# Optimization experiments

Hardware: AMD Instinct MI355X
Metric: run time of the kernel (lower is better)

Reference implementation:

```python
import jax, jax.numpy as jnp
import numpy as np

B = 64        # number of graph segments
BASE = 384    # mean verts per segment
LMAX = 512    # pad length (counts in [256, 512])
H_DIM = 256
H_DIV = 128   # h_dim // h_dim_div
HEADS = 4
DH = H_DIV // HEADS  # 32


def _counts(seed):
    rng = np.random.default_rng(seed)
    d = rng.integers(-128, 129, B)
    d[1::2] = -d[::2]            # paired so the total is exactly B*BASE
    return (BASE + d).astype(np.int64)


def _pad_indices(counts, L):
    # Gather indices/mask mapping packed ragged tokens -> padded [B, L].
    counts = np.asarray(counts)
    off = np.concatenate([[0], np.cumsum(counts)[:-1]])
    ar = np.arange(L)[None, :]
    mask = ar < counts[:, None]
    idx = np.where(mask, off[:, None] + ar, 0)
    return idx, mask


def setup_inputs() -> dict:
    key = jax.random.key(0)
    ks = jax.random.split(key, 16)
    src_num_verts = _counts(0)
    dst_num_verts = _counts(1)
    total = B * BASE  # 24576 for both src and dst

    def w(k, shape):
        return 0.02 * jax.random.normal(k, shape, jnp.float32)

    return {
        'src_h': jax.random.normal(ks[0], (total, H_DIM), jnp.float32),
        'dst_h': jax.random.normal(ks[1], (total, H_DIM), jnp.float32),
        'src_num_verts': src_num_verts,
        'dst_num_verts': dst_num_verts,
        # 1x1 Conv1d == linear over channels
        'Wq': w(ks[2], (H_DIV, H_DIM)), 'bq': w(ks[3], (H_DIV,)),
        'Wk': w(ks[4], (H_DIV, H_DIM)), 'bk': w(ks[5], (H_DIV,)),
        'Wv': w(ks[6], (H_DIV, H_DIM)), 'bv': w(ks[7], (H_DIV,)),
        'Wm': w(ks[8], (H_DIV, H_DIV)), 'bm': w(ks[9], (H_DIV,)),
        'W1': w(ks[10], (H_DIM, H_DIM + H_DIV)), 'b1': w(ks[11], (H_DIM,)),
        'g1': 1.0 + 0.1 * jax.random.normal(ks[12], (H_DIM,), jnp.float32),
        'be1': w(ks[13], (H_DIM,)),
        'rm1': w(ks[14], (H_DIM,)),
        'rv1': jax.random.uniform(ks[15], (H_DIM,), jnp.float32, 0.5, 1.5),
        'W2': w(jax.random.fold_in(key, 100), (H_DIM, H_DIM)),
        'b2': w(jax.random.fold_in(key, 101), (H_DIM,)),
        'g2': 1.0 + 0.1 * jax.random.normal(jax.random.fold_in(key, 102), (H_DIM,), jnp.float32),
        'be2': w(jax.random.fold_in(key, 103), (H_DIM,)),
        'rm2': w(jax.random.fold_in(key, 104), (H_DIM,)),
        'rv2': jax.random.uniform(jax.random.fold_in(key, 105), (H_DIM,), jnp.float32, 0.5, 1.5),
    }


def _bn(x, g, b, rm, rv):
    # BatchNorm1d in eval mode (running stats)
    return (x - rm) / jnp.sqrt(rv + 1e-5) * g + b


def reference(src_h, dst_h, src_num_verts, dst_num_verts,
              Wq, bq, Wk, bk, Wv, bv, Wm, bm,
              W1, b1, g1, be1, rm1, rv1,
              W2, b2, g2, be2, rm2, rv2):
    didx, dmask = _pad_indices(dst_num_verts, LMAX)
    sidx, smask = _pad_indices(src_num_verts, LMAX)

    # fused projections over all packed tokens (1x1 conv == matmul)
    q = src_h_proj = dst_h @ Wq.T + bq        # [Nd, H_DIV]
    k = src_h @ Wk.T + bk                     # [Ns, H_DIV]
    v = src_h @ Wv.T + bv

    # pad to block-diagonal batched form; channel c = d*HEADS + h per torch view
    qp = q[didx].reshape(B, LMAX, DH, HEADS)
    kp = k[sidx].reshape(B, LMAX, DH, HEADS)
    vp = v[sidx].reshape(B, LMAX, DH, HEADS)

    scores = jnp.einsum('bndh,bmdh->bhnm', qp, kp) / (DH ** 0.5)
    scores = jnp.where(jnp.asarray(smask)[:, None, None, :], scores, -1e9)
    attn = jax.nn.softmax(scores, axis=-1)
    msg = jnp.einsum('bhnm,bmdh->bndh', attn, vp).reshape(B, LMAX, H_DIV)
    msg = msg @ Wm.T + bm                     # merge conv

    bb, ii = np.nonzero(dmask)                # unpad back to packed layout
    h_msg = msg[bb, ii]                       # [Nd, H_DIV]

    x = jnp.concatenate([dst_h, h_msg], axis=-1)
    x = _bn(x @ W1.T + b1, g1, be1, rm1, rv1)
    x = jax.nn.relu(x)
    x = _bn(x @ W2.T + b2, g2, be2, rm2, rv2)
    return dst_h + x
```

## Files before the change

kernel.cpp:

```cpp
#include <hip/hip_runtime.h>
#include <hip/hip_bf16.h>
#include <math.h>

#define B_SEG 64
#define HDIM 256
#define HDIV 128
#define NHEADS 4
#define DH 32
#define KSTR 40
#define VSTR 520
#define PSTR 136
#define QSC 0.17677669529663687f

typedef unsigned short u16;
typedef unsigned int u32;

typedef __attribute__((ext_vector_type(8))) short s8v;
typedef __attribute__((ext_vector_type(4))) float f4v;

__device__ __forceinline__ u16 f2bf(float f) {
    u32 v;
    __builtin_memcpy(&v, &f, 4);
    u32 r = v + 0x7fffu + ((v >> 16) & 1u);
    return (u16)(r >> 16);
}

__device__ __forceinline__ void async_cp16(const u16* g, u16* l) {
    __builtin_amdgcn_global_load_lds(
        (const __attribute__((address_space(1))) u32*)g,
        (__attribute__((address_space(3))) u32*)l, 16, 0, 0);
}

__global__ __launch_bounds__(256) void k_prep(
    const float* __restrict__ Wq, const float* __restrict__ bq,
    const float* __restrict__ Wk, const float* __restrict__ bk,
    const float* __restrict__ Wv, const float* __restrict__ bv,
    const float* __restrict__ Wm, const float* __restrict__ bm,
    const float* __restrict__ W1, const float* __restrict__ b1,
    const float* __restrict__ g1, const float* __restrict__ be1,
    const float* __restrict__ rm1, const float* __restrict__ rv1,
    const float* __restrict__ W2, const float* __restrict__ b2,
    const float* __restrict__ g2, const float* __restrict__ be2,
    const float* __restrict__ rm2, const float* __restrict__ rv2,
    const int* __restrict__ sc_raw, const int* __restrict__ dc_raw,
    const float* __restrict__ src_h, const float* __restrict__ dst_h,
    int* __restrict__ meta,
    u16* __restrict__ pWq, u16* __restrict__ pWkv,
    u16* __restrict__ pW1f, u16* __restrict__ pW2,
    float* __restrict__ bqp, float* __restrict__ bkvp,
    float* __restrict__ sc1, float* __restrict__ sh1,
    float* __restrict__ sc2, float* __restrict__ sh2,
    u16* __restrict__ srcb, u16* __restrict__ dstb, int ntot) {
    if (blockIdx.x < 1028) {
        int idx = blockIdx.x * 256 + threadIdx.x;
        if (idx < 32768) {
            int cp = idx >> 8, k = idx & 255;
            int c = ((cp & 31) << 2) | (cp >> 5);
            pWq[idx] = f2bf(Wq[c * 256 + k]);
        } else if (idx < 98304) {
            int i = idx - 32768;
            int rp = i >> 8, k = i & 255;
            int r = rp & 127;
            int c = ((r & 31) << 2) | (r >> 5);
            float v = (rp < 128) ? Wk[c * 256 + k] : Wv[c * 256 + k];
            pWkv[i] = f2bf(v);
        } else if (idx < 163840) {
            int i = idx - 98304;
            int o = i >> 8, k = i & 255;
            pW1f[o * 384 + k] = f2bf(W1[o * 384 + k]);
        } else if (idx < 196608) {
            int i = idx - 163840;
            int o = i >> 7, cp = i & 127;
            int c = ((cp & 31) << 2) | (cp >> 5);
            float acc = 0.f;
            for (int j = 0; j < 128; j++)
                acc += W1[o * 384 + 256 + j] * Wm[j * 128 + c];
            pW1f[o * 384 + 256 + cp] = f2bf(acc);
        } else if (idx < 262144) {
            int i = idx - 196608;
            pW2[i] = f2bf(W2[i]);
        } else if (idx < 263168) {
            int p = idx - 262144;
            if (p < 128) {
                int c = ((p & 31) << 2) | (p >> 5);
                bqp[p] = bq[c] * QSC;
            } else if (p < 384) {
                int r = p - 128; int rr = r & 127;
                int c = ((rr & 31) << 2) | (rr >> 5);
                bkvp[r] = (r < 128) ? bk[c] : bv[c];
            } else if (p < 640) {
                int o = p - 384;
                float bsum = 0.f;
                for (int j = 0; j < 128; j++)
                    bsum += W1[o * 384 + 256 + j] * bm[j];
                float s = g1[o] * rsqrtf(rv1[o] + 1e-5f);
                sc1[o] = s;
                sh1[o] = (b1[o] + bsum - rm1[o]) * s + be1[o];
            } else if (p < 896) {
                int o = p - 640;
                float s = g2[o] * rsqrtf(rv2[o] + 1e-5f);
                sc2[o] = s;
                sh2[o] = (b2[o] - rm2[o]) * s + be2[o];
            }
        }
    } else if (blockIdx.x == 1028) {
        if (threadIdx.x == 0) {
            bool is64 = (sc_raw[1] == 0);
            int so = 0, dofs = 0;
            for (int i = 0; i < B_SEG; i++) {
                int s = is64 ? sc_raw[2 * i] : sc_raw[i];
                int d = is64 ? dc_raw[2 * i] : dc_raw[i];
                meta[i] = s; meta[64 + i] = d;
                meta[128 + i] = so; meta[192 + i] = dofs;
                so += s; dofs += d;
            }
        }
    } else {
        int i = (blockIdx.x - 1029) * 256 + threadIdx.x;
        int half = ntot * 64;
        const float4* s;
        u16* o;
        int j = i;
        if (i < half) { s = (const float4*)src_h; o = srcb; }
        else { s = (const float4*)dst_h; o = dstb; j = i - half; }
        float4 v = s[j];
        ushort4 u = {f2bf(v.x), f2bf(v.y), f2bf(v.z), f2bf(v.w)};
        ((ushort4*)o)[j] = u;
    }
}

__device__ __forceinline__ void gemm_body(
    const u16* __restrict__ A, int lda,
    const u16* __restrict__ A2, int lda2, int K1,
    const u16* __restrict__ Bw, int K, int m0, int n0,
    const float* __restrict__ scale, const float* __restrict__ shift,
    const float* __restrict__ resid,
    void* __restrict__ Cout, int ldc, int flags,
    u16* Al, u16* Bl) {
    int tid = threadIdx.x;
    int w = tid >> 6, lane = tid & 63;
    int wm = w & 1, wn = w >> 1;
    int l15 = lane & 15, quad = lane >> 4;
    int srow = w * 32 + (lane >> 2);
    int scol = (lane & 3) << 3;
    u16* al0 = Al + w * 1024;
    u16* bl0 = Bl + w * 1024;
    f4v acc[4][4] = {};

    for (int k0 = 0; k0 < K; k0 += 32) {
        const u16* Ag; int aL, acol;
        if (k0 < K1) { Ag = A; aL = lda; acol = k0; }
        else { Ag = A2; aL = lda2; acol = k0 - K1; }
        async_cp16(&Ag[(size_t)(m0 + srow) * aL + acol + scol], al0);
        async_cp16(&Ag[(size_t)(m0 + srow + 16) * aL + acol + scol], al0 + 512);
        async_cp16(&Bw[(size_t)(n0 + srow) * K + k0 + scol], bl0);
        async_cp16(&Bw[(size_t)(n0 + srow + 16) * K + k0 + scol], bl0 + 512);
        __syncthreads();
        s8v af[4], bf[4];
#pragma unroll
        for (int i = 0; i < 4; i++)
            af[i] = *(const s8v*)(&Al[(wm * 64 + i * 16 + l15) * 32 + quad * 8]);
#pragma unroll
        for (int j = 0; j < 4; j++)
            bf[j] = *(const s8v*)(&Bl[(wn * 64 + j * 16 + l15) * 32 + quad * 8]);
#pragma unroll
        for (int i = 0; i < 4; i++)
#pragma unroll
            for (int j = 0; j < 4; j++)
                acc[i][j] = __builtin_amdgcn_mfma_f32_16x16x32_bf16(
                    af[i], bf[j], acc[i][j], 0, 0, 0);
        __syncthreads();
    }
#pragma unroll
    for (int i = 0; i < 4; i++) {
#pragma unroll
        for (int j = 0; j < 4; j++) {
            int n = n0 + wn * 64 + j * 16 + l15;
            float sc = scale ? scale[n] : 1.f;
            float sh = shift ? shift[n] : 0.f;
#pragma unroll
            for (int r = 0; r < 4; r++) {
                int m = m0 + wm * 64 + i * 16 + quad * 4 + r;
                float v = acc[i][j][r];
                if (flags & 4) v *= QSC;
                v = v * sc + sh;
                if (flags & 1) v = fmaxf(v, 0.f);
                if (resid) v += resid[(size_t)m * 256 + n];
                if (flags & 2) ((float*)Cout)[(size_t)m * ldc + n] = v;
                else ((u16*)Cout)[(size_t)m * ldc + n] = f2bf(v);
            }
        }
    }
}

__global__ __launch_bounds__(256) void k_qkv(
    const u16* __restrict__ dstb, const u16* __restrict__ srcb,
    const u16* __restrict__ pWq, const u16* __restrict__ pWkv,
    const float* __restrict__ bqp, const float* __restrict__ bkvp,
    u16* __restrict__ qb, u16* __restrict__ kvb) {
    __shared__ u16 Al[4096];
    __shared__ u16 Bl[4096];
    int m0 = blockIdx.x * 128;
    if (blockIdx.y == 0)
        gemm_body(dstb, 256, dstb, 256, 256, pWq, 256, m0, 0,
                  nullptr, bqp, nullptr, qb, 128, 4, Al, Bl);
    else
        gemm_body(srcb, 256, srcb, 256, 256, pWkv, 256, m0, (blockIdx.y - 1) * 128,
                  nullptr, bkvp, nullptr, kvb, 256, 0, Al, Bl);
}

__global__ __launch_bounds__(256) void k_gemm(
    const u16* __restrict__ A, int lda,
    const u16* __restrict__ A2, int lda2, int K1,
    const u16* __restrict__ Bw, int K,
    const float* __restrict__ scale, const float* __restrict__ shift,
    const float* __restrict__ resid,
    void* __restrict__ Cout, int ldc, int flags) {
    __shared__ u16 Al[4096];
    __shared__ u16 Bl[4096];
    gemm_body(A, lda, A2, lda2, K1, Bw, K, blockIdx.x * 128, blockIdx.y * 128,
              scale, shift, resid, Cout, ldc, flags, Al, Bl);
}

__global__ __launch_bounds__(512, 2) void k_attn(
    const u16* __restrict__ qb, const u16* __restrict__ kvb,
    const int* __restrict__ meta, u16* __restrict__ msgb) {
    extern __shared__ u16 sm[];
    u16* Kl = sm;
    u16* Vl = sm + 512 * KSTR;
    u16* Pl = Vl + 32 * VSTR;
    int b = blockIdx.x, h = blockIdx.y;
    int ns = meta[b], nd = meta[64 + b];
    int soff = meta[128 + b], doff = meta[192 + b];
    int tid = threadIdx.x, w = tid >> 6, lane = tid & 63;
    int l15 = lane & 15, quad = lane >> 4;

    {
        int m = tid;
        if (m < ns) {
            const uint4* ks = (const uint4*)&kvb[(size_t)(soff + m) * 256 + h * 32];
#pragma unroll
            for (int q4 = 0; q4 < 4; q4++)
                *(uint4*)&Kl[m * KSTR + q4 * 8] = ks[q4];
            uint4 vv[4];
            const uint4* vs = (const uint4*)&kvb[(size_t)(soff + m) * 256 + 128 + h * 32];
#pragma unroll
            for (int q4 = 0; q4 < 4; q4++) vv[q4] = vs[q4];
            const u16* pv = (const u16*)vv;
#pragma unroll
            for (int d = 0; d < 32; d++) Vl[d * VSTR + m] = pv[d];
        } else {
#pragma unroll
            for (int d = 0; d < 32; d++) Vl[d * VSTR + m] = 0;
        }
    }
    __syncthreads();

    int nt = (ns + 15) >> 4;
    int nc = (ns + 127) >> 7;
    u16* Pw = Pl + w * 16 * PSTR;

    for (int s0 = w * 16; s0 < nd; s0 += 128) {
        int qr = min(s0 + l15, nd - 1);
        s8v aq = *(const s8v*)&qb[(size_t)(doff + qr) * 128 + h * 32 + quad * 8];

        f4v e[32];
        float lsum[4] = {0.f, 0.f, 0.f, 0.f};
#pragma unroll
        for (int t = 0; t < 32; t++) {
            if (t < nt) {
                int kr = t * 16 + l15;
                s8v bk = *(const s8v*)&Kl[kr * KSTR + quad * 8];
                f4v s_ = __builtin_amdgcn_mfma_f32_16x16x32_bf16(
                    aq, bk, (f4v){0.f, 0.f, 0.f, 0.f}, 0, 0, 0);
                bool ok = kr < ns;
#pragma unroll
                for (int r = 0; r < 4; r++) {
                    float ev = ok ? __expf(s_[r]) : 0.f;
                    e[t][r] = ev;
                    lsum[r] += ev;
                }
            } else {
#pragma unroll
                for (int r = 0; r < 4; r++) e[t][r] = 0.f;
            }
        }
        float inv[4];
#pragma unroll
        for (int r = 0; r < 4; r++) {
            float s_ = lsum[r];
#pragma unroll
            for (int x = 1; x < 16; x <<= 1) s_ += __shfl_xor(s_, x, 16);
            inv[r] = 1.f / s_;
        }

        f4v oa0 = {0.f, 0.f, 0.f, 0.f}, oa1 = {0.f, 0.f, 0.f, 0.f};
#pragma unroll
        for (int c = 0; c < 4; c++) {
            if (c < nc) {
#pragma unroll
                for (int tt = 0; tt < 8; tt++)
#pragma unroll
                    for (int r = 0; r < 4; r++)
                        Pw[(quad * 4 + r) * PSTR + tt * 16 + l15] =
                            f2bf(e[c * 8 + tt][r]);
#pragma unroll
                for (int kc = 0; kc < 4; kc++) {
                    s8v ap = *(const s8v*)&Pw[l15 * PSTR + kc * 32 + quad * 8];
                    s8v bv0 = *(const s8v*)&Vl[l15 * VSTR + c * 128 + kc * 32 + quad * 8];
                    s8v bv1 = *(const s8v*)&Vl[(16 + l15) * VSTR + c * 128 + kc * 32 + quad * 8];
                    oa0 = __builtin_amdgcn_mfma_f32_16x16x32_bf16(ap, bv0, oa0, 0, 0, 0);
                    oa1 = __builtin_amdgcn_mfma_f32_16x16x32_bf16(ap, bv1, oa1, 0, 0, 0);
                }
            }
        }
#pragma unroll
        for (int r = 0; r < 4; r++) {
            int row = s0 + quad * 4 + r;
            if (row < nd) {
                size_t base = (size_t)(doff + row) * 128 + h * 32;
                msgb[base + l15] = f2bf(oa0[r] * inv[r]);
                msgb[base + 16 + l15] = f2bf(oa1[r] * inv[r]);
            }
        }
    }
}

extern "C" void kernel_launch(void* const* d_in, const int* in_sizes, int n_in,
                              void* d_out, int out_size, void* d_ws, size_t ws_size,
                              hipStream_t stream) {
    const float* src_h = (const float*)d_in[0];
    const float* dst_h = (const float*)d_in[1];
    const int* snv = (const int*)d_in[2];
    const int* dnv = (const int*)d_in[3];
    const float* Wq = (const float*)d_in[4];  const float* bq = (const float*)d_in[5];
    const float* Wk = (const float*)d_in[6];  const float* bk = (const float*)d_in[7];
    const float* Wv = (const float*)d_in[8];  const float* bv = (const float*)d_in[9];
    const float* Wm = (const float*)d_in[10]; const float* bm = (const float*)d_in[11];
    const float* W1 = (const float*)d_in[12]; const float* b1 = (const float*)d_in[13];
    const float* g1 = (const float*)d_in[14]; const float* be1 = (const float*)d_in[15];
    const float* rm1 = (const float*)d_in[16]; const float* rv1 = (const float*)d_in[17];
    const float* W2 = (const float*)d_in[18]; const float* b2 = (const float*)d_in[19];
    const float* g2 = (const float*)d_in[20]; const float* be2 = (const float*)d_in[21];
    const float* rm2 = (const float*)d_in[22]; const float* rv2 = (const float*)d_in[23];

    int ntot = out_size / HDIM;
    int mt = ntot / 128;

    char* ws = (char*)d_ws;
    int* meta = (int*)ws;
    float* bqp = (float*)(ws + 4096);
    float* bkvp = (float*)(ws + 4608);
    float* sc1 = (float*)(ws + 6144);
    float* sh1 = (float*)(ws + 7168);
    float* sc2 = (float*)(ws + 8192);
    float* sh2 = (float*)(ws + 9216);
    u16* pWq = (u16*)(ws + 16384);
    u16* pWkv = (u16*)(ws + 81920);
    u16* pW1f = (u16*)(ws + 212992);
    u16* pW2 = (u16*)(ws + 409600);
    u16* srcb = (u16*)(ws + 1048576);
    u16* x1b = srcb;
    u16* dstb = (u16*)(ws + 13631488);

    u16* qb = (u16*)d_out;
    u16* kvb = qb + (size_t)ntot * 128;
    u16* msgb = kvb + (size_t)ntot * 256;

    hipFuncSetAttribute((const void*)k_attn,
                        hipFuncAttributeMaxDynamicSharedMemorySize, 131072);

    k_prep<<<dim3(1029 + ntot / 2), dim3(256), 0, stream>>>(
        Wq, bq, Wk, bk, Wv, bv, Wm, bm, W1, b1, g1, be1, rm1, rv1,
        W2, b2, g2, be2, rm2, rv2, snv, dnv, src_h, dst_h, meta,
        pWq, pWkv, pW1f, pW2, bqp, bkvp, sc1, sh1, sc2, sh2,
        srcb, dstb, ntot);
    k_qkv<<<dim3(mt, 3), dim3(256), 0, stream>>>(
        dstb, srcb, pWq, pWkv, bqp, bkvp, qb, kvb);
    k_attn<<<dim3(B_SEG, NHEADS), dim3(512), 109056, stream>>>(qb, kvb, meta, msgb);
    k_gemm<<<dim3(mt, 2), dim3(256), 0, stream>>>(
        dstb, 256, msgb, 128, 256, pW1f, 384, sc1, sh1, nullptr, x1b, 256, 1);
    k_gemm<<<dim3(mt, 2), dim3(256), 0, stream>>>(
        x1b, 256, x1b, 256, 256, pW2, 256, sc2, sh2, dst_h, d_out, 256, 2);
}
```

Baseline: 235.6 us.

## Split attention across query halves, stream K from global, widen GEMM K-step

The attention kernel gains a third grid dimension that splits each segment's query tiles across two blocks. K is no longer staged in LDS and is read directly from global memory, which shrinks shared memory so more blocks fit per CU. The score, exp and PV work is fused per 128-key chunk, so only 8 score tiles stay live in registers instead of 32. Separately, the GEMM body now loads a 64-wide K slab per barrier pair to halve synchronisations, at the cost of doubling its LDS footprint.

```diff
diff --git a/kernel.cpp b/kernel.cpp
--- a/kernel.cpp
+++ b/kernel.cpp
@@ -7,7 +7,6 @@
 #define HDIV 128
 #define NHEADS 4
 #define DH 32
-#define KSTR 40
 #define VSTR 520
 #define PSTR 136
 #define QSC 0.17677669529663687f
@@ -141,34 +140,40 @@
     int w = tid >> 6, lane = tid & 63;
     int wm = w & 1, wn = w >> 1;
     int l15 = lane & 15, quad = lane >> 4;
-    int srow = w * 32 + (lane >> 2);
-    int scol = (lane & 3) << 3;
-    u16* al0 = Al + w * 1024;
-    u16* bl0 = Bl + w * 1024;
+    int srow = w * 32 + (lane >> 3);
+    int scol = (lane & 7) << 3;
     f4v acc[4][4] = {};
 
-    for (int k0 = 0; k0 < K; k0 += 32) {
+    for (int k0 = 0; k0 < K; k0 += 64) {
         const u16* Ag; int aL, acol;
         if (k0 < K1) { Ag = A; aL = lda; acol = k0; }
         else { Ag = A2; aL = lda2; acol = k0 - K1; }
-        async_cp16(&Ag[(size_t)(m0 + srow) * aL + acol + scol], al0);
-        async_cp16(&Ag[(size_t)(m0 + srow + 16) * aL + acol + scol], al0 + 512);
-        async_cp16(&Bw[(size_t)(n0 + srow) * K + k0 + scol], bl0);
-        async_cp16(&Bw[(size_t)(n0 + srow + 16) * K + k0 + scol], bl0 + 512);
+#pragma unroll
+        for (int j = 0; j < 4; j++) {
+            async_cp16(&Ag[(size_t)(m0 + srow + j * 8) * aL + acol + scol],
+                       Al + w * 2048 + j * 512);
+            async_cp16(&Bw[(size_t)(n0 + srow + j * 8) * K + k0 + scol],
+                       Bl + w * 2048 + j * 512);
+        }
         __syncthreads();
-        s8v af[4], bf[4];
-#pragma unroll
-        for (int i = 0; i < 4; i++)
-            af[i] = *(const s8v*)(&Al[(wm * 64 + i * 16 + l15) * 32 + quad * 8]);
-#pragma unroll
-        for (int j = 0; j < 4; j++)
-            bf[j] = *(const s8v*)(&Bl[(wn * 64 + j * 16 + l15) * 32 + quad * 8]);
-#pragma unroll
-        for (int i = 0; i < 4; i++)
+#pragma unroll
+        for (int kk = 0; kk < 2; kk++) {
+            s8v af[4], bf[4];
+#pragma unroll
+            for (int i = 0; i < 4; i++)
+                af[i] = *(const s8v*)(&Al[(wm * 64 + i * 16 + l15) * 64
+                                          + kk * 32 + quad * 8]);
 #pragma unroll
             for (int j = 0; j < 4; j++)
-                acc[i][j] = __builtin_amdgcn_mfma_f32_16x16x32_bf16(
-                    af[i], bf[j], acc[i][j], 0, 0, 0);
+                bf[j] = *(const s8v*)(&Bl[(wn * 64 + j * 16 + l15) * 64
+                                          + kk * 32 + quad * 8]);
+#pragma unroll
+            for (int i = 0; i < 4; i++)
+#pragma unroll
+                for (int j = 0; j < 4; j++)
+                    acc[i][j] = __builtin_amdgcn_mfma_f32_16x16x32_bf16(
+                        af[i], bf[j], acc[i][j], 0, 0, 0);
+        }
         __syncthreads();
     }
 #pragma unroll
@@ -198,8 +203,8 @@
     const u16* __restrict__ pWq, const u16* __restrict__ pWkv,
     const float* __restrict__ bqp, const float* __restrict__ bkvp,
     u16* __restrict__ qb, u16* __restrict__ kvb) {
-    __shared__ u16 Al[4096];
-    __shared__ u16 Bl[4096];
+    __shared__ u16 Al[8192];
+    __shared__ u16 Bl[8192];
     int m0 = blockIdx.x * 128;
     if (blockIdx.y == 0)
         gemm_body(dstb, 256, dstb, 256, 256, pWq, 256, m0, 0,
@@ -216,20 +221,19 @@
     const float* __restrict__ scale, const float* __restrict__ shift,
     const float* __restrict__ resid,
     void* __restrict__ Cout, int ldc, int flags) {
-    __shared__ u16 Al[4096];
-    __shared__ u16 Bl[4096];
+    __shared__ u16 Al[8192];
+    __shared__ u16 Bl[8192];
     gemm_body(A, lda, A2, lda2, K1, Bw, K, blockIdx.x * 128, blockIdx.y * 128,
               scale, shift, resid, Cout, ldc, flags, Al, Bl);
 }
 
-__global__ __launch_bounds__(512, 2) void k_attn(
+__global__ __launch_bounds__(512, 4) void k_attn(
     const u16* __restrict__ qb, const u16* __restrict__ kvb,
     const int* __restrict__ meta, u16* __restrict__ msgb) {
     extern __shared__ u16 sm[];
-    u16* Kl = sm;
-    u16* Vl = sm + 512 * KSTR;
-    u16* Pl = Vl + 32 * VSTR;
-    int b = blockIdx.x, h = blockIdx.y;
+    u16* Vl = sm;
+    u16* Pl = sm + 32 * VSTR;
+    int b = blockIdx.x, h = blockIdx.y, z = blockIdx.z;
     int ns = meta[b], nd = meta[64 + b];
     int soff = meta[128 + b], doff = meta[192 + b];
     int tid = threadIdx.x, w = tid >> 6, lane = tid & 63;
@@ -238,12 +242,9 @@
     {
         int m = tid;
         if (m < ns) {
-            const uint4* ks = (const uint4*)&kvb[(size_t)(soff + m) * 256 + h * 32];
-#pragma unroll
-            for (int q4 = 0; q4 < 4; q4++)
-                *(uint4*)&Kl[m * KSTR + q4 * 8] = ks[q4];
             uint4 vv[4];
-            const uint4* vs = (const uint4*)&kvb[(size_t)(soff + m) * 256 + 128 + h * 32];
+            const uint4* vs =
+                (const uint4*)&kvb[(size_t)(soff + m) * 256 + 128 + h * 32];
 #pragma unroll
             for (int q4 = 0; q4 < 4; q4++) vv[q4] = vs[q4];
             const u16* pv = (const u16*)vv;
@@ -256,54 +257,43 @@
     }
     __syncthreads();
 
-    int nt = (ns + 15) >> 4;
     int nc = (ns + 127) >> 7;
     u16* Pw = Pl + w * 16 * PSTR;
-
-    for (int s0 = w * 16; s0 < nd; s0 += 128) {
+    const u16* kb = kvb + h * 32;
+
+    for (int s0 = (z * 8 + w) * 16; s0 < nd; s0 += 256) {
         int qr = min(s0 + l15, nd - 1);
         s8v aq = *(const s8v*)&qb[(size_t)(doff + qr) * 128 + h * 32 + quad * 8];
 
-        f4v e[32];
         float lsum[4] = {0.f, 0.f, 0.f, 0.f};
-#pragma unroll
-        for (int t = 0; t < 32; t++) {
-            if (t < nt) {
-                int kr = t * 16 + l15;
-                s8v bk = *(const s8v*)&Kl[kr * KSTR + quad * 8];
-                f4v s_ = __builtin_amdgcn_mfma_f32_16x16x32_bf16(
-                    aq, bk, (f4v){0.f, 0.f, 0.f, 0.f}, 0, 0, 0);
-                bool ok = kr < ns;
-#pragma unroll
-                for (int r = 0; r < 4; r++) {
-                    float ev = ok ? __expf(s_[r]) : 0.f;
-                    e[t][r] = ev;
-                    lsum[r] += ev;
-                }
-            } else {
-#pragma unroll
-                for (int r = 0; r < 4; r++) e[t][r] = 0.f;
-            }
-        }
-        float inv[4];
-#pragma unroll
-        for (int r = 0; r < 4; r++) {
-            float s_ = lsum[r];
-#pragma unroll
-            for (int x = 1; x < 16; x <<= 1) s_ += __shfl_xor(s_, x, 16);
-            inv[r] = 1.f / s_;
-        }
-
         f4v oa0 = {0.f, 0.f, 0.f, 0.f}, oa1 = {0.f, 0.f, 0.f, 0.f};
 #pragma unroll
         for (int c = 0; c < 4; c++) {
             if (c < nc) {
+                f4v e[8];
+#pragma unroll
+                for (int tt = 0; tt < 8; tt++) {
+                    int kr = min(c * 128 + tt * 16 + l15, ns - 1);
+                    s8v bk = *(const s8v*)&kb[(size_t)(soff + kr) * 256 + quad * 8];
+                    e[tt] = __builtin_amdgcn_mfma_f32_16x16x32_bf16(
+                        aq, bk, (f4v){0.f, 0.f, 0.f, 0.f}, 0, 0, 0);
+                }
+#pragma unroll
+                for (int tt = 0; tt < 8; tt++) {
+                    bool ok = (c * 128 + tt * 16 + l15) < ns;
+#pragma unroll
+                    for (int r = 0; r < 4; r++) {
+                        float ev = ok ? __expf(e[tt][r]) : 0.f;
+                        e[tt][r] = ev;
+                        lsum[r] += ev;
+                    }
+                }
 #pragma unroll
                 for (int tt = 0; tt < 8; tt++)
 #pragma unroll
                     for (int r = 0; r < 4; r++)
                         Pw[(quad * 4 + r) * PSTR + tt * 16 + l15] =
-                            f2bf(e[c * 8 + tt][r]);
+                            f2bf(e[tt][r]);
 #pragma unroll
                 for (int kc = 0; kc < 4; kc++) {
                     s8v ap = *(const s8v*)&Pw[l15 * PSTR + kc * 32 + quad * 8];
@@ -313,6 +303,14 @@
                     oa1 = __builtin_amdgcn_mfma_f32_16x16x32_bf16(ap, bv1, oa1, 0, 0, 0);
                 }
             }
+        }
+        float inv[4];
+#pragma unroll
+        for (int r = 0; r < 4; r++) {
+            float s_ = lsum[r];
+#pragma unroll
+            for (int x = 1; x < 16; x <<= 1) s_ += __shfl_xor(s_, x, 16);
+            inv[r] = 1.f / s_;
         }
 #pragma unroll
         for (int r = 0; r < 4; r++) {
@@ -377,7 +375,8 @@
         srcb, dstb, ntot);
     k_qkv<<<dim3(mt, 3), dim3(256), 0, stream>>>(
         dstb, srcb, pWq, pWkv, bqp, bkvp, qb, kvb);
-    k_attn<<<dim3(B_SEG, NHEADS), dim3(512), 109056, stream>>>(qb, kvb, meta, msgb);
+    k_attn<<<dim3(B_SEG, NHEADS, 2), dim3(512), 68096, stream>>>(
+        qb, kvb, meta, msgb);
     k_gemm<<<dim3(mt, 2), dim3(256), 0, stream>>>(
         dstb, 256, msgb, 128, 256, pW1f, 384, sc1, sh1, nullptr, x1b, 256, 1);
     k_gemm<<<dim3(mt, 2), dim3(256), 0, stream>>>(
```

After: 238.9 us. Within noise of the previous version (+1.4%).
